# Optimization experiments

Hardware: AMD Instinct MI355X
Metric: run time of the kernel (lower is better)

The kernel has to match this reference:

```python
import jax, jax.numpy as jnp
import numpy as np
from jax import lax

B, C, T = 16, 1, 2097152
DS = 16  # downsample_factor


def setup_inputs() -> dict:
    key = jax.random.key(0)
    audio = jax.random.normal(key, (B, C, T), dtype=jnp.float32) * 0.5
    sr, attack_ms, release_ms = 44100.0, 10.0, 100.0
    tc = float(np.exp(-np.log10(9.0)))  # exp(-log10(9)) time-constant numerator
    return {
        'audio': audio,
        'threshold': jnp.array([-20.0], jnp.float32),
        'ratio': jnp.array([4.0], jnp.float32),
        'makeup': jnp.array([3.0], jnp.float32),
        'attack_time': jnp.array([tc / (sr * attack_ms * 0.001 * DS)], jnp.float32),
        'release_time': jnp.array([tc / (sr * release_ms * 0.001 * DS)], jnp.float32),
    }


def _linear_downsample(x, factor):
    # F.interpolate(mode='linear', align_corners=False, scale_factor=1/factor)
    Tin = x.shape[-1]
    Tout = Tin // factor
    scale = Tin / Tout
    src = (jnp.arange(Tout, dtype=jnp.float32) + 0.5) * scale - 0.5
    src = jnp.clip(src, 0.0, Tin - 1)
    x0 = jnp.floor(src).astype(jnp.int32)
    x1 = jnp.minimum(x0 + 1, Tin - 1)
    w = src - x0.astype(jnp.float32)
    return x[..., x0] * (1.0 - w) + x[..., x1] * w


def _upsample_with_windows(x, up):
    # x: [B, C, F] framewise envelope; overlap-add with periodic Hann, hop=up
    xb = jnp.concatenate([x, x[..., -1:]], axis=-1)  # add endpoint
    n = jnp.arange(2 * up, dtype=jnp.float32)
    win = 0.5 * (1.0 - jnp.cos(2.0 * jnp.pi * n / (2 * up)))  # torch.hann_window (periodic)
    frames = xb[..., None] * win  # [B, C, F+1, 2*up]
    bsz, ch, nf, fl = frames.shape
    L = (nf - 1) * up + fl
    idx = (jnp.arange(nf)[:, None] * up + jnp.arange(fl)[None, :]).reshape(-1)
    out = jnp.zeros((bsz, ch, L), frames.dtype).at[:, :, idx].add(frames.reshape(bsz, ch, -1))
    return out[:, :, up:-up]


def reference(audio, threshold, ratio, makeup, attack_time, release_time):
    audio_db = 20.0 * jnp.log10(jnp.abs(audio) + 1e-8)
    comp_db = jnp.where(audio_db > threshold,
                        threshold + (audio_db - threshold) / ratio,
                        audio_db)
    gain = comp_db - audio_db  # [B, C, T], static gain reduction in dB (<= 0)
    gd = _linear_downsample(gain, DS)  # [B, C, T//DS]
    # sequential attack/release gain smoothing (one-pole recurrence) over frames
    gd_t = jnp.moveaxis(gd, -1, 0)  # [T//DS, B, C]
    def step(prev, tgt):
        new = jnp.where(tgt >= prev,
                        attack_time * prev + (1.0 - attack_time) * tgt,
                        release_time * prev + (1.0 - release_time) * tgt)
        return new, new
    _, ys = lax.scan(step, gd_t[0], gd_t)
    gs = jnp.moveaxis(ys, 0, -1)  # smoothed gain, [B, C, T//DS]
    gup = _upsample_with_windows(gs, DS)[..., :gain.shape[-1]]
    out_db = audio_db + gup + makeup
    out = 10.0 ** (out_db / 20.0)
    return jnp.where(audio < 0, -out, out)
```

## Files before the change

kernel.cpp:

```cpp
#include <hip/hip_runtime.h>
#include <math.h>

#define B_SZ 16
#define T_LEN 2097152
#define F_LEN (T_LEN / 16)
#define NFRAMES (B_SZ * F_LEN)
#define NV4 (B_SZ * T_LEN / 4)
#define CHUNK 16
#define WARM 16

__global__ __launch_bounds__(256) void k_gain_ds(const float4* __restrict__ audio4,
                                                 const float* __restrict__ thr_p,
                                                 const float* __restrict__ ratio_p,
                                                 float* __restrict__ gd) {
    int i = blockIdx.x * 256 + threadIdx.x;
    float thr = thr_p[0];
    float slope = 1.0f / ratio_p[0] - 1.0f;
    float4 f = audio4[i];
    int pos = i & 3;
    float v = (pos == 1) ? f.w : f.x;
    float a = fabsf(v) + 1e-8f;
    float db = 6.0205999132796239f * __log2f(a);
    float over = db - thr;
    float g = over > 0.0f ? over * slope : 0.0f;
    float gp = __shfl_xor(g, 3);
    if (pos == 1)
        gd[i >> 2] = 0.5f * (g + gp);
}

__global__ __launch_bounds__(256) void k_scan(const float* __restrict__ gd,
                                              const float* __restrict__ at_p,
                                              const float* __restrict__ rt_p,
                                              float* __restrict__ gs) {
    int idx = blockIdx.x * 256 + threadIdx.x;
    const int CPB = F_LEN / CHUNK;
    int b = idx >> 13;
    int c = idx & (CPB - 1);
    float at = at_p[0], rt = rt_p[0];
    const float* gdb = gd + (size_t)b * F_LEN;
    float* gsb = gs + (size_t)b * F_LEN;
    int c0 = c << 4;
    bool first = (c == 0);
    int s = first ? 0 : (c0 - WARM);

    float v[WARM + CHUNK];
    const float4* p = reinterpret_cast<const float4*>(gdb + s);
#pragma unroll
    for (int i = 0; i < (WARM + CHUNK) / 4; ++i)
        reinterpret_cast<float4*>(v)[i] = p[i];

    float o[CHUNK];
    float y;
    if (first) {
        y = v[0];
        o[0] = y;
#pragma unroll
        for (int i = 1; i < CHUNK; ++i) {
            float t = v[i];
            y = fmaf((t >= y) ? at : rt, y - t, t);
            o[i] = y;
        }
    } else {
        y = v[0];
#pragma unroll
        for (int i = 1; i < WARM; ++i) {
            float t = v[i];
            y = fmaf((t >= y) ? at : rt, y - t, t);
        }
#pragma unroll
        for (int i = 0; i < CHUNK; ++i) {
            float t = v[WARM + i];
            y = fmaf((t >= y) ? at : rt, y - t, t);
            o[i] = y;
        }
    }
    float4* q = reinterpret_cast<float4*>(gsb + c0);
#pragma unroll
    for (int i = 0; i < CHUNK / 4; ++i)
        q[i] = reinterpret_cast<float4*>(o)[i];
}

__global__ __launch_bounds__(256) void k_out(const float4* __restrict__ audio4,
                                             const float* __restrict__ gs,
                                             const float* __restrict__ mk_p,
                                             float4* __restrict__ out4) {
    int i = blockIdx.x * 256 + threadIdx.x;
    int t0 = i << 2;
    int b = t0 >> 21;
    int t = t0 & (T_LEN - 1);
    int q = t >> 4;
    int r0 = t & 15;
    const float* gsb = gs + (size_t)b * F_LEN;
    float gq = gsb[q];
    int q1 = q + 1; if (q1 > F_LEN - 1) q1 = F_LEN - 1;
    float d = gsb[q1] - gq;
    float mk = mk_p[0];
    const float K = 0.16609640474436813f;
    float4 x = audio4[i];
    float xs[4] = {x.x, x.y, x.z, x.w};
    float os[4];
#pragma unroll
    for (int j = 0; j < 4; ++j) {
        float cs = __cosf((float)(r0 + j) * 0.19634954084936207f);
        float wl = 0.5f - 0.5f * cs;
        float gup = fmaf(d, wl, gq);
        float m = fabsf(xs[j]) + 1e-8f;
        float v = m * __builtin_amdgcn_exp2f((gup + mk) * K);
        os[j] = (xs[j] < 0.0f) ? -v : v;
    }
    out4[i] = make_float4(os[0], os[1], os[2], os[3]);
}

extern "C" void kernel_launch(void* const* d_in, const int* in_sizes, int n_in,
                              void* d_out, int out_size, void* d_ws, size_t ws_size,
                              hipStream_t stream) {
    const float* audio  = (const float*)d_in[0];
    const float* thr    = (const float*)d_in[1];
    const float* ratio  = (const float*)d_in[2];
    const float* makeup = (const float*)d_in[3];
    const float* at     = (const float*)d_in[4];
    const float* rt     = (const float*)d_in[5];
    float* out = (float*)d_out;

    float* gd = (float*)d_ws;
    float* gs = gd + NFRAMES;

    k_gain_ds<<<NV4 / 256, 256, 0, stream>>>((const float4*)audio, thr, ratio, gd);

    int nthreads = B_SZ * (F_LEN / CHUNK);
    k_scan<<<nthreads / 256, 256, 0, stream>>>(gd, at, rt, gs);

    k_out<<<NV4 / 256, 256, 0, stream>>>((const float4*)audio, gs, makeup, (float4*)out);
}
```

Measured before the change: 258.6 us.

## Fuse gain downsampling into scan kernel and emit paired envelope samples

Drops the separate gain/downsample kernel. The scan kernel now gathers the two audio samples per frame (indices 7 and 8) straight from audio and computes the gain in dB inline. The scan writes (g[q], g[q+1]) pairs so the output kernel does one float2 load instead of two scalar loads, and the makeup term is folded into a single fma. This removes a full read pass over the audio and one launch, but the scan threads now make strided scalar gathers with 64-byte stride, and each thread recomputes the log for its 16-frame warm-up, which doubles the transcendental work there.

After: 274.9 us. 6.3% more time.

```diff
diff --git a/kernel.cpp b/kernel.cpp
--- a/kernel.cpp
+++ b/kernel.cpp
@@ -4,84 +4,82 @@
 #define B_SZ 16
 #define T_LEN 2097152
 #define F_LEN (T_LEN / 16)
-#define NFRAMES (B_SZ * F_LEN)
+#define CHUNK 16
+#define CPB (F_LEN / CHUNK)
+#define NCHUNKS (B_SZ * CPB)
 #define NV4 (B_SZ * T_LEN / 4)
-#define CHUNK 16
-#define WARM 16
+#define PRE 16
 
-__global__ __launch_bounds__(256) void k_gain_ds(const float4* __restrict__ audio4,
-                                                 const float* __restrict__ thr_p,
-                                                 const float* __restrict__ ratio_p,
-                                                 float* __restrict__ gd) {
-    int i = blockIdx.x * 256 + threadIdx.x;
-    float thr = thr_p[0];
-    float slope = 1.0f / ratio_p[0] - 1.0f;
-    float4 f = audio4[i];
-    int pos = i & 3;
-    float v = (pos == 1) ? f.w : f.x;
-    float a = fabsf(v) + 1e-8f;
-    float db = 6.0205999132796239f * __log2f(a);
-    float over = db - thr;
-    float g = over > 0.0f ? over * slope : 0.0f;
-    float gp = __shfl_xor(g, 3);
-    if (pos == 1)
-        gd[i >> 2] = 0.5f * (g + gp);
+__device__ __forceinline__ float gain_db(float s, float thr, float slope) {
+    float db = 6.0205999132796239f * __log2f(fabsf(s) + 1e-8f);
+    float ov = db - thr;
+    return ov > 0.0f ? ov * slope : 0.0f;
 }
 
-__global__ __launch_bounds__(256) void k_scan(const float* __restrict__ gd,
+__global__ __launch_bounds__(256) void k_scan(const float* __restrict__ audio,
+                                              const float* __restrict__ thr_p,
+                                              const float* __restrict__ ratio_p,
                                               const float* __restrict__ at_p,
                                               const float* __restrict__ rt_p,
-                                              float* __restrict__ gs) {
+                                              float2* __restrict__ gsp) {
     int idx = blockIdx.x * 256 + threadIdx.x;
-    const int CPB = F_LEN / CHUNK;
     int b = idx >> 13;
     int c = idx & (CPB - 1);
-    float at = at_p[0], rt = rt_p[0];
-    const float* gdb = gd + (size_t)b * F_LEN;
-    float* gsb = gs + (size_t)b * F_LEN;
     int c0 = c << 4;
-    bool first = (c == 0);
-    int s = first ? 0 : (c0 - WARM);
+    const float* Af = audio + (size_t)b * T_LEN;
+    const float thr   = thr_p[0];
+    const float slope = 1.0f / ratio_p[0] - 1.0f;
 
-    float v[WARM + CHUNK];
-    const float4* p = reinterpret_cast<const float4*>(gdb + s);
+    float g[PRE + CHUNK + 1];
 #pragma unroll
-    for (int i = 0; i < (WARM + CHUNK) / 4; ++i)
-        reinterpret_cast<float4*>(v)[i] = p[i];
+    for (int i = 0; i < PRE + CHUNK + 1; ++i) {
+        int f = c0 - PRE + i;
+        f = f < 0 ? 0 : (f > F_LEN - 1 ? F_LEN - 1 : f);
+        float t7 = Af[(size_t)f * 16 + 7];
+        float t8 = Af[(size_t)f * 16 + 8];
+        g[i] = 0.5f * (gain_db(t7, thr, slope) + gain_db(t8, thr, slope));
+    }
 
-    float o[CHUNK];
+    const float at = at_p[0], rt = rt_p[0];
+    float o[CHUNK + 1];
     float y;
-    if (first) {
-        y = v[0];
+    if (c == 0) {
+        y = g[PRE];
         o[0] = y;
 #pragma unroll
-        for (int i = 1; i < CHUNK; ++i) {
-            float t = v[i];
+        for (int i = 1; i < CHUNK + 1; ++i) {
+            float t = g[PRE + i];
             y = fmaf((t >= y) ? at : rt, y - t, t);
             o[i] = y;
         }
     } else {
-        y = v[0];
+        y = g[0];
 #pragma unroll
-        for (int i = 1; i < WARM; ++i) {
-            float t = v[i];
+        for (int i = 1; i < PRE; ++i) {
+            float t = g[i];
             y = fmaf((t >= y) ? at : rt, y - t, t);
         }
 #pragma unroll
-        for (int i = 0; i < CHUNK; ++i) {
-            float t = v[WARM + i];
+        for (int i = 0; i < CHUNK + 1; ++i) {
+            float t = g[PRE + i];
             y = fmaf((t >= y) ? at : rt, y - t, t);
             o[i] = y;
         }
     }
-    float4* q = reinterpret_cast<float4*>(gsb + c0);
+    if (c == CPB - 1) o[CHUNK] = o[CHUNK - 1];
+
+    float2 pr[CHUNK];
 #pragma unroll
-    for (int i = 0; i < CHUNK / 4; ++i)
-        q[i] = reinterpret_cast<float4*>(o)[i];
+    for (int i = 0; i < CHUNK; ++i)
+        pr[i] = make_float2(o[i], o[i + 1]);
+    float4* q4 = reinterpret_cast<float4*>(gsp + (size_t)b * F_LEN + c0);
+#pragma unroll
+    for (int i = 0; i < CHUNK / 2; ++i)
+        q4[i] = reinterpret_cast<float4*>(pr)[i];
 }
 
 __global__ __launch_bounds__(256) void k_out(const float4* __restrict__ audio4,
-                                             const float* __restrict__ gs,
+                                             const float2* __restrict__ gsp,
                                              const float* __restrict__ mk_p,
                                              float4* __restrict__ out4) {
     int i = blockIdx.x * 256 + threadIdx.x;
@@ -90,22 +88,21 @@
     int t = t0 & (T_LEN - 1);
     int q = t >> 4;
     int r0 = t & 15;
-    const float* gsb = gs + (size_t)b * F_LEN;
-    float gq = gsb[q];
-    int q1 = q + 1; if (q1 > F_LEN - 1) q1 = F_LEN - 1;
-    float d = gsb[q1] - gq;
-    float mk = mk_p[0];
-    const float K = 0.16609640474436813f;
+    float2 gp = gsp[(size_t)b * F_LEN + q];
+    float gq = gp.x;
+    float d  = gp.y - gp.x;
+    const float K   = 0.16609640474436813f;
+    const float mkK = mk_p[0] * K;
     float4 x = audio4[i];
     float xs[4] = {x.x, x.y, x.z, x.w};
     float os[4];
 #pragma unroll
     for (int j = 0; j < 4; ++j) {
-        float cs = __cosf((float)(r0 + j) * 0.19634954084936207f);
-        float wl = 0.5f - 0.5f * cs;
+        float cs  = __cosf((float)(r0 + j) * 0.19634954084936207f);
+        float wl  = 0.5f - 0.5f * cs;
         float gup = fmaf(d, wl, gq);
-        float m = fabsf(xs[j]) + 1e-8f;
-        float v = m * __builtin_amdgcn_exp2f((gup + mk) * K);
+        float m   = fabsf(xs[j]) + 1e-8f;
+        float v   = m * __builtin_amdgcn_exp2f(fmaf(gup, K, mkK));
         os[j] = (xs[j] < 0.0f) ? -v : v;
     }
     out4[i] = make_float4(os[0], os[1], os[2], os[3]);
@@ -122,13 +119,9 @@
     const float* rt     = (const float*)d_in[5];
     float* out = (float*)d_out;
 
-    float* gd = (float*)d_ws;
-    float* gs = gd + NFRAMES;
+    float2* gsp = (float2*)d_ws;
 
-    k_gain_ds<<<NV4 / 256, 256, 0, stream>>>((const float4*)audio, thr, ratio, gd);
-
-    int nthreads = B_SZ * (F_LEN / CHUNK);
-    k_scan<<<nthreads / 256, 256, 0, stream>>>(gd, at, rt, gs);
-
-    k_out<<<NV4 / 256, 256, 0, stream>>>((const float4*)audio, gs, makeup, (float4*)out);
+    k_scan<<<NCHUNKS / 256, 256, 0, stream>>>(audio, thr, ratio, at, rt, gsp);
+    k_out<<<NV4 / 256, 256, 0, stream>>>((const float4*)audio, gsp, makeup,
+                                         (float4*)out);
 }
```
